# Performance work log

Measured on AMD Instinct MI355X. Metric: run time of the kernel, lower is better.

The kernel has to match this reference:

```python
import jax, jax.numpy as jnp
import numpy as np


def setup_inputs() -> dict:
    key = jax.random.key(0)
    k1, k2, k3 = jax.random.split(key, 3)
    R, N, F_IN, F_OUT = 8, 4096, 128, 128
    adjacency = jax.random.uniform(k1, (R, N, N), dtype=jnp.float32)
    features = jax.random.normal(k2, (N, F_IN), dtype=jnp.float32)
    weight = jax.random.uniform(k3, (R, F_OUT, F_IN), dtype=jnp.float32)
    return {"adjacency": adjacency, "features": features, "weight": weight}


def reference(adjacency, features, weight):
    # Original: y = sum_r A_r @ X @ W_r^T
    # Batched over relations: msg[r] = A_r @ X  -> [R, N, F_in]
    msg = jnp.einsum('rnm,mf->rnf', adjacency, features)
    # Project per-relation and reduce over relations: [N, F_out]
    y = jnp.einsum('rnf,rof->no', msg, weight)
    return y
```

## Files before the change

### kernel.cpp

```cpp
#include <hip/hip_runtime.h>
#include <hip/hip_bf16.h>


#define NN 4096
#define FF 128
#define RR 8
#define KSPLIT 2

typedef __attribute__((ext_vector_type(4))) float  f32x4;
typedef __attribute__((ext_vector_type(8))) __bf16 bf16x8;
typedef __attribute__((ext_vector_type(4))) short  s16x4;

union Frag { unsigned u[4]; bf16x8 v; };

__device__ __forceinline__ unsigned pk2bf(float a, float b) {
  unsigned ua = __builtin_bit_cast(unsigned, a);
  unsigned ub = __builtin_bit_cast(unsigned, b);
  ua = (ua + (((ua >> 16) & 1u) + 0x7fffu)) >> 16;
  ub = (ub + (((ub >> 16) & 1u) + 0x7fffu)) >> 16;
  return ua | (ub << 16);
}

__device__ __forceinline__ unsigned short f2bf(float a) {
  unsigned ua = __builtin_bit_cast(unsigned, a);
  return (unsigned short)((ua + (((ua >> 16) & 1u) + 0x7fffu)) >> 16);
}

__device__ __forceinline__ void cvt_frag(Frag& f, const f32x4& x0, const f32x4& x1) {
  f.u[0] = pk2bf(x0.x, x0.y);
  f.u[1] = pk2bf(x0.z, x0.w);
  f.u[2] = pk2bf(x1.x, x1.y);
  f.u[3] = pk2bf(x1.z, x1.w);
}

__global__ __launch_bounds__(256, 2)
void zt_kernel(const float* __restrict__ X, const float* __restrict__ W,
               unsigned short* __restrict__ Zt) {
  const int lane = threadIdx.x & 63;
  const int wave = threadIdx.x >> 6;
  const int quad = lane >> 4;
  const int l16  = lane & 15;
  const int m0   = blockIdx.x * 128 + wave * 32;
  const int r    = blockIdx.y;
  const float* Wr = W + (size_t)r * FF * FF;

  f32x4 acc[2][8] = {};

  #pragma unroll
  for (int k = 0; k < FF; k += 32) {
    Frag a[2], b[8];
    #pragma unroll
    for (int mt = 0; mt < 2; ++mt) {
      const float* p = X + (size_t)(m0 + mt * 16 + l16) * FF + k + quad * 8;
      f32x4 x0 = *(const f32x4*)p;
      f32x4 x1 = *(const f32x4*)(p + 4);
      cvt_frag(a[mt], x0, x1);
    }
    #pragma unroll
    for (int nt = 0; nt < 8; ++nt) {
      const float* p = Wr + (size_t)(nt * 16 + l16) * FF + k + quad * 8;
      f32x4 x0 = *(const f32x4*)p;
      f32x4 x1 = *(const f32x4*)(p + 4);
      cvt_frag(b[nt], x0, x1);
    }
    #pragma unroll
    for (int mt = 0; mt < 2; ++mt)
      #pragma unroll
      for (int nt = 0; nt < 8; ++nt)
        acc[mt][nt] = __builtin_amdgcn_mfma_f32_16x16x32_bf16(
            a[mt].v, b[nt].v, acc[mt][nt], 0, 0, 0);
  }

  unsigned short* Zr = Zt + (size_t)r * FF * NN;
  #pragma unroll
  for (int mt = 0; mt < 2; ++mt)
    #pragma unroll
    for (int nt = 0; nt < 8; ++nt) {
      const int o = nt * 16 + l16;
      const int m = m0 + mt * 16 + quad * 4;
      s16x4 v;
      v.x = (short)f2bf(acc[mt][nt].x);
      v.y = (short)f2bf(acc[mt][nt].y);
      v.z = (short)f2bf(acc[mt][nt].z);
      v.w = (short)f2bf(acc[mt][nt].w);
      *(s16x4*)(Zr + (size_t)o * NN + m) = v;
    }
}

__global__ __launch_bounds__(256, 2)
void rgcn_main(const float* __restrict__ A, const unsigned short* __restrict__ Zt,
               float* __restrict__ out) {
  const int lane = threadIdx.x & 63;
  const int wave = threadIdx.x >> 6;
  const int quad = lane >> 4;
  const int l16  = lane & 15;
  const int m0   = blockIdx.x * 128 + wave * 32;
  const int r    = blockIdx.y;
  const int k0   = blockIdx.z * (NN / KSPLIT);

  const float* Ar = A + (size_t)r * NN * NN;
  const unsigned short* Zr = Zt + (size_t)r * FF * NN;

  const float* pa0 = Ar + (size_t)(m0 + l16) * NN + quad * 8 + k0;
  const float* pa1 = Ar + (size_t)(m0 + 16 + l16) * NN + quad * 8 + k0;
  const unsigned short* pb[8];
  #pragma unroll
  for (int nt = 0; nt < 8; ++nt)
    pb[nt] = Zr + (size_t)(nt * 16 + l16) * NN + quad * 8 + k0;

  f32x4 acc[2][8] = {};

  #pragma unroll 2
  for (int k = 0; k < NN / KSPLIT; k += 32) {
    Frag a[2];
    {
      f32x4 x0 = *(const f32x4*)(pa0 + k);
      f32x4 x1 = *(const f32x4*)(pa0 + k + 4);
      cvt_frag(a[0], x0, x1);
      f32x4 y0 = *(const f32x4*)(pa1 + k);
      f32x4 y1 = *(const f32x4*)(pa1 + k + 4);
      cvt_frag(a[1], y0, y1);
    }
    bf16x8 b[8];
    #pragma unroll
    for (int nt = 0; nt < 8; ++nt)
      b[nt] = *(const bf16x8*)(pb[nt] + k);

    #pragma unroll
    for (int mt = 0; mt < 2; ++mt)
      #pragma unroll
      for (int nt = 0; nt < 8; ++nt)
        acc[mt][nt] = __builtin_amdgcn_mfma_f32_16x16x32_bf16(
            a[mt].v, b[nt], acc[mt][nt], 0, 0, 0);
  }

  #pragma unroll
  for (int mt = 0; mt < 2; ++mt)
    #pragma unroll
    for (int nt = 0; nt < 8; ++nt) {
      const int col = nt * 16 + l16;
      const int row = m0 + mt * 16 + quad * 4;
      unsafeAtomicAdd(&out[(size_t)(row + 0) * FF + col], acc[mt][nt].x);
      unsafeAtomicAdd(&out[(size_t)(row + 1) * FF + col], acc[mt][nt].y);
      unsafeAtomicAdd(&out[(size_t)(row + 2) * FF + col], acc[mt][nt].z);
      unsafeAtomicAdd(&out[(size_t)(row + 3) * FF + col], acc[mt][nt].w);
    }
}

extern "C" void kernel_launch(void* const* d_in, const int* in_sizes, int n_in,
                              void* d_out, int out_size, void* d_ws, size_t ws_size,
                              hipStream_t stream) {
  const float* A = (const float*)d_in[0];
  const float* X = (const float*)d_in[1];
  const float* W = (const float*)d_in[2];
  float* out = (float*)d_out;
  unsigned short* Zt = (unsigned short*)d_ws;

  hipMemsetAsync(d_out, 0, (size_t)out_size * sizeof(float), stream);
  zt_kernel<<<dim3(NN / 128, RR), 256, 0, stream>>>(X, W, Zt);
  rgcn_main<<<dim3(NN / 128, RR, KSPLIT), 256, 0, stream>>>(A, Zt, out);
}
```

Measured before the change: 794.4 us.

## Replace atomic output accumulation with partial buffers and a separate reduce kernel

The main kernel now writes each split's partial tile to a workspace buffer in MFMA fragment order, and a new reduce kernel sums the 32 partials and scatters them into the output. This removes the float atomics and the output memset. The split-K factor rises to 4, relation is moved into blockIdx.x, the A loads are software-prefetched one iteration ahead, and bf16 conversion uses the native vector convert. The cost is a 64 MB partial buffer that must be written and read back, plus an extra launch.

```diff
diff --git a/kernel.cpp b/kernel.cpp
--- a/kernel.cpp
+++ b/kernel.cpp
@@ -5,13 +5,23 @@
 #define NN 4096
 #define FF 128
 #define RR 8
-#define KSPLIT 2
+#define KSPLIT 4
+#define CHUNK (NN / KSPLIT)
+#define ITERS (CHUNK / 32)
+#define NPART (RR * KSPLIT)
+#define PELEMS (NN * FF)
 
 typedef __attribute__((ext_vector_type(4))) float  f32x4;
 typedef __attribute__((ext_vector_type(8))) __bf16 bf16x8;
+typedef __attribute__((ext_vector_type(4))) __bf16 bf16x4;
 typedef __attribute__((ext_vector_type(4))) short  s16x4;
 
 union Frag { unsigned u[4]; bf16x8 v; };
+
+__device__ __forceinline__ bf16x8 cvt8(f32x4 x0, f32x4 x1) {
+  return __builtin_convertvector(
+      __builtin_shufflevector(x0, x1, 0, 1, 2, 3, 4, 5, 6, 7), bf16x8);
+}
 
 __device__ __forceinline__ unsigned pk2bf(float a, float b) {
   unsigned ua = __builtin_bit_cast(unsigned, a);
@@ -20,12 +30,10 @@
   ub = (ub + (((ub >> 16) & 1u) + 0x7fffu)) >> 16;
   return ua | (ub << 16);
 }
-
 __device__ __forceinline__ unsigned short f2bf(float a) {
   unsigned ua = __builtin_bit_cast(unsigned, a);
   return (unsigned short)((ua + (((ua >> 16) & 1u) + 0x7fffu)) >> 16);
 }
-
 __device__ __forceinline__ void cvt_frag(Frag& f, const f32x4& x0, const f32x4& x1) {
   f.u[0] = pk2bf(x0.x, x0.y);
   f.u[1] = pk2bf(x0.z, x0.w);
@@ -52,16 +60,12 @@
     #pragma unroll
     for (int mt = 0; mt < 2; ++mt) {
       const float* p = X + (size_t)(m0 + mt * 16 + l16) * FF + k + quad * 8;
-      f32x4 x0 = *(const f32x4*)p;
-      f32x4 x1 = *(const f32x4*)(p + 4);
-      cvt_frag(a[mt], x0, x1);
+      cvt_frag(a[mt], *(const f32x4*)p, *(const f32x4*)(p + 4));
     }
     #pragma unroll
     for (int nt = 0; nt < 8; ++nt) {
       const float* p = Wr + (size_t)(nt * 16 + l16) * FF + k + quad * 8;
-      f32x4 x0 = *(const f32x4*)p;
-      f32x4 x1 = *(const f32x4*)(p + 4);
-      cvt_frag(b[nt], x0, x1);
+      cvt_frag(b[nt], *(const f32x4*)p, *(const f32x4*)(p + 4));
     }
     #pragma unroll
     for (int mt = 0; mt < 2; ++mt)
@@ -87,64 +91,85 @@
     }
 }
 
-__global__ __launch_bounds__(256, 2)
+__global__ __launch_bounds__(256, 3)
 void rgcn_main(const float* __restrict__ A, const unsigned short* __restrict__ Zt,
-               float* __restrict__ out) {
-  const int lane = threadIdx.x & 63;
-  const int wave = threadIdx.x >> 6;
-  const int quad = lane >> 4;
-  const int l16  = lane & 15;
-  const int m0   = blockIdx.x * 128 + wave * 32;
-  const int r    = blockIdx.y;
-  const int k0   = blockIdx.z * (NN / KSPLIT);
+               float* __restrict__ P) {
+  const int lane  = threadIdx.x & 63;
+  const int wave  = threadIdx.x >> 6;
+  const int quad  = lane >> 4;
+  const int l16   = lane & 15;
+  const int r     = blockIdx.x & 7;
+  const int mtile = blockIdx.x >> 3;
+  const int ks    = blockIdx.y;
+  const int m0    = mtile * 128 + wave * 32;
+  const int k0    = ks * CHUNK;
 
   const float* Ar = A + (size_t)r * NN * NN;
   const unsigned short* Zr = Zt + (size_t)r * FF * NN;
 
   const float* pa0 = Ar + (size_t)(m0 + l16) * NN + quad * 8 + k0;
-  const float* pa1 = Ar + (size_t)(m0 + 16 + l16) * NN + quad * 8 + k0;
-  const unsigned short* pb[8];
-  #pragma unroll
-  for (int nt = 0; nt < 8; ++nt)
-    pb[nt] = Zr + (size_t)(nt * 16 + l16) * NN + quad * 8 + k0;
+  const float* pa1 = pa0 + (size_t)16 * NN;
+  const unsigned short* pb = Zr + (size_t)l16 * NN + quad * 8 + k0;
 
   f32x4 acc[2][8] = {};
 
+  f32x4 nx0 = *(const f32x4*)(pa0);
+  f32x4 nx1 = *(const f32x4*)(pa0 + 4);
+  f32x4 ny0 = *(const f32x4*)(pa1);
+  f32x4 ny1 = *(const f32x4*)(pa1 + 4);
+
   #pragma unroll 2
-  for (int k = 0; k < NN / KSPLIT; k += 32) {
-    Frag a[2];
-    {
-      f32x4 x0 = *(const f32x4*)(pa0 + k);
-      f32x4 x1 = *(const f32x4*)(pa0 + k + 4);
-      cvt_frag(a[0], x0, x1);
-      f32x4 y0 = *(const f32x4*)(pa1 + k);
-      f32x4 y1 = *(const f32x4*)(pa1 + k + 4);
-      cvt_frag(a[1], y0, y1);
-    }
+  for (int it = 0; it < ITERS; ++it) {
+    const int k = it * 32;
     bf16x8 b[8];
     #pragma unroll
     for (int nt = 0; nt < 8; ++nt)
-      b[nt] = *(const bf16x8*)(pb[nt] + k);
+      b[nt] = *(const bf16x8*)(pb + (size_t)nt * 16 * NN + k);
+
+    f32x4 cx0 = nx0, cx1 = nx1, cy0 = ny0, cy1 = ny1;
+    if (it + 1 < ITERS) {
+      nx0 = *(const f32x4*)(pa0 + k + 32);
+      nx1 = *(const f32x4*)(pa0 + k + 36);
+      ny0 = *(const f32x4*)(pa1 + k + 32);
+      ny1 = *(const f32x4*)(pa1 + k + 36);
+    }
+
+    bf16x8 a0 = cvt8(cx0, cx1);
+    bf16x8 a1 = cvt8(cy0, cy1);
 
     #pragma unroll
-    for (int mt = 0; mt < 2; ++mt)
-      #pragma unroll
-      for (int nt = 0; nt < 8; ++nt)
-        acc[mt][nt] = __builtin_amdgcn_mfma_f32_16x16x32_bf16(
-            a[mt].v, b[nt], acc[mt][nt], 0, 0, 0);
+    for (int nt = 0; nt < 8; ++nt)
+      acc[0][nt] = __builtin_amdgcn_mfma_f32_16x16x32_bf16(a0, b[nt], acc[0][nt], 0, 0, 0);
+    #pragma unroll
+    for (int nt = 0; nt < 8; ++nt)
+      acc[1][nt] = __builtin_amdgcn_mfma_f32_16x16x32_bf16(a1, b[nt], acc[1][nt], 0, 0, 0);
   }
 
+  const int p   = r * KSPLIT + ks;
+  const int gbw = mtile * 4 + wave;
+  float* Pp = P + ((size_t)(p * 128 + gbw) * 16) * 256;
   #pragma unroll
   for (int mt = 0; mt < 2; ++mt)
     #pragma unroll
-    for (int nt = 0; nt < 8; ++nt) {
-      const int col = nt * 16 + l16;
-      const int row = m0 + mt * 16 + quad * 4;
-      unsafeAtomicAdd(&out[(size_t)(row + 0) * FF + col], acc[mt][nt].x);
-      unsafeAtomicAdd(&out[(size_t)(row + 1) * FF + col], acc[mt][nt].y);
-      unsafeAtomicAdd(&out[(size_t)(row + 2) * FF + col], acc[mt][nt].z);
-      unsafeAtomicAdd(&out[(size_t)(row + 3) * FF + col], acc[mt][nt].w);
-    }
+    for (int nt = 0; nt < 8; ++nt)
+      *(f32x4*)(Pp + (mt * 8 + nt) * 256 + lane * 4) = acc[mt][nt];
+}
+
+__global__ __launch_bounds__(256)
+void reduce_kernel(const float* __restrict__ P, float* __restrict__ out) {
+  const int t = blockIdx.x * 256 + threadIdx.x;
+  float s = 0.f;
+  #pragma unroll
+  for (int p = 0; p < NPART; ++p) s += P[(size_t)p * PELEMS + t];
+  const int reg  = t & 3;
+  const int lane = (t >> 2) & 63;
+  const int inst = (t >> 8) & 15;
+  const int gbw  = t >> 12;
+  const int quad = lane >> 4, l16 = lane & 15;
+  const int mt   = inst >> 3, nt = inst & 7;
+  const int row  = gbw * 32 + mt * 16 + quad * 4 + reg;
+  const int col  = nt * 16 + l16;
+  out[(size_t)row * FF + col] = s;
 }
 
 extern "C" void kernel_launch(void* const* d_in, const int* in_sizes, int n_in,
@@ -154,9 +179,11 @@
   const float* X = (const float*)d_in[1];
   const float* W = (const float*)d_in[2];
   float* out = (float*)d_out;
+
   unsigned short* Zt = (unsigned short*)d_ws;
+  float* P = (float*)((char*)d_ws + (size_t)RR * FF * NN * 2);
 
-  hipMemsetAsync(d_out, 0, (size_t)out_size * sizeof(float), stream);
   zt_kernel<<<dim3(NN / 128, RR), 256, 0, stream>>>(X, W, Zt);
-  rgcn_main<<<dim3(NN / 128, RR, KSPLIT), 256, 0, stream>>>(A, Zt, out);
+  rgcn_main<<<dim3(32 * RR, KSPLIT), 256, 0, stream>>>(A, Zt, P);
+  reduce_kernel<<<dim3(PELEMS / 256), 256, 0, stream>>>(P, out);
 }
```

After: 815.4 us. 1.03x slower.
